# Optimization experiments

Hardware: AMD Instinct MI355X
Metric: run time of the kernel (lower is better)

Reference implementation:

```python
import jax, jax.numpy as jnp
import numpy as np

N_DOCS, DOC_LEN, H = 10000, 200, 128   # document token vectors [N, d, h]
B, QLEN, NPIDS = 16, 32, 500           # batch, query tokens, candidate pids per query
TOPK = 100


def setup_inputs() -> dict:
    key = jax.random.key(0)
    k1, k2, k3 = jax.random.split(key, 3)
    q_vectors = jax.random.normal(k1, (B, QLEN, H), dtype=jnp.float32)
    vectors = jax.random.normal(k2, (N_DOCS, DOC_LEN, H), dtype=jnp.float32)
    pids = jax.random.randint(k3, (B, NPIDS), 0, N_DOCS, dtype=jnp.int32)
    boundaries = jnp.array([0, N_DOCS], dtype=jnp.int32)
    return {"q_vectors": q_vectors, "pids": pids, "vectors": vectors,
            "boundaries": boundaries, "k": TOPK}


def _dedupe_row(row):
    # torch.unique-like: sort ascending, replace duplicate entries with -1.
    # (Original pads each row's unique set with -1; only tie-order in the
    #  downstream top-k can differ, the score/pid sets are identical.)
    s = jnp.sort(row)
    dup = jnp.concatenate([jnp.zeros((1,), dtype=bool), s[1:] == s[:-1]])
    return jnp.where(dup, jnp.int32(-1), s)


def reference(q_vectors, pids, vectors, boundaries, k):
    lo = boundaries[0]
    n_vec = vectors.shape[0]
    pids = pids - lo
    pids = jnp.where((pids < 0) | (pids >= n_vec), jnp.int32(-1), pids)
    pids = jax.vmap(_dedupe_row)(pids)                       # [b, K]

    # gather doc token vectors (pid == -1 wraps to last doc; masked below,
    # matching torch's vectors[pids] semantics for -1)
    d_vectors = vectors[pids]                                # [b, K, d, h]
    scores = jnp.einsum('bqh,bkdh->bkqd', q_vectors, d_vectors)
    scores = scores.max(axis=-1).sum(axis=-1)                # MaxSim: max over doc tokens, sum over query tokens -> [b, K]
    scores = jnp.where(pids < 0, -jnp.inf, scores)

    top_scores, top_idx = jax.lax.top_k(scores, k)           # sorted descending
    top_pids = jnp.take_along_axis(pids, top_idx, axis=-1)
    top_pids = jnp.where(top_pids >= 0, top_pids + lo, top_pids)
    return top_scores, top_pids
```

## Files before the change

### kernel.cpp

```cpp
#include <hip/hip_runtime.h>
#include <float.h>
#include <limits.h>

#define NB     16
#define QLEN   32
#define HDIM   128
#define NPIDS  500
#define NDOCS  10000
#define DLEN   200
#define TOPK   100
#define VROW   (DLEN * HDIM)

typedef _Float16 f16x8 __attribute__((ext_vector_type(8)));
typedef float    f32x16 __attribute__((ext_vector_type(16)));

__global__ __launch_bounds__(512) void dedupe_kernel(const int* __restrict__ pids,
                                                     const int* __restrict__ boundaries,
                                                     int* __restrict__ dpids) {
    __shared__ int s[512];
    const int b = blockIdx.x;
    const int t = threadIdx.x;
    const int lo = boundaries[0];

    int v = INT_MAX;
    if (t < NPIDS) {
        int p = pids[b * NPIDS + t] - lo;
        if (p < 0 || p >= NDOCS) p = -1;
        v = p;
    }
    s[t] = v;
    __syncthreads();

    for (int k = 2; k <= 512; k <<= 1) {
        for (int j = k >> 1; j > 0; j >>= 1) {
            int ixj = t ^ j;
            if (ixj > t) {
                int a = s[t], c = s[ixj];
                bool up = ((t & k) == 0);
                if ((a > c) == up) { s[t] = c; s[ixj] = a; }
            }
            __syncthreads();
        }
    }

    if (t < NPIDS) {
        int val = s[t];
        int o = val;
        if (val == INT_MAX) o = -1;
        else if (t > 0 && val == s[t - 1]) o = -1;
        dpids[b * NPIDS + t] = o;
    }
}

__device__ __forceinline__ void split2h(float a, _Float16& h, _Float16& m) {
    h = (_Float16)a;
    float r = a - (float)h;
    m = (_Float16)r;
}

__device__ __forceinline__ void split2h_pack8(const float4 c0, const float4 c1,
                                              f16x8& H, f16x8& M) {
    float f[8] = {c0.x, c0.y, c0.z, c0.w, c1.x, c1.y, c1.z, c1.w};
    f16x8 Ht, Mt;
    #pragma unroll
    for (int j = 0; j < 8; ++j) {
        _Float16 hh, mm;
        split2h(f[j], hh, mm);
        Ht[j] = hh; Mt[j] = mm;
    }
    H = Ht; M = Mt;
}

__global__ __launch_bounds__(256, 3) void score_kernel(const float* __restrict__ qv,
                                                       const float* __restrict__ vectors,
                                                       const int* __restrict__ dpids,
                                                       float* __restrict__ scores) {
    const int t    = threadIdx.x;
    const int w    = t >> 6;
    const int lane = t & 63;
    const int row  = lane & 31;
    const int half = lane >> 5;

    const int cbase = (blockIdx.x * 4 + w) * 2;
    const int b     = cbase / NPIDS;

    f16x8 qh[8], qm[8];
    {
        const float* qb = qv + ((size_t)b * QLEN + row) * HDIM + half * 8;
        #pragma unroll
        for (int ks = 0; ks < 8; ++ks) {
            const float4 a0 = *(const float4*)(qb + ks * 16);
            const float4 a1 = *(const float4*)(qb + ks * 16 + 4);
            split2h_pack8(a0, a1, qh[ks], qm[ks]);
        }
    }

    for (int ci = 0; ci < 2; ++ci) {
        const int c   = cbase + ci;
        const int pid = dpids[c];
        if (pid < 0) {
            if (lane == 0) scores[c] = -__builtin_inff();
            continue;
        }

        const float* vb = vectors + (size_t)pid * VROW + half * 8;

        float rmax[16];
        #pragma unroll
        for (int j = 0; j < 16; ++j) rmax[j] = -FLT_MAX;

        const float* vt0 = vb + (size_t)row * HDIM;
        float4 pf[4][2];
        #pragma unroll
        for (int s = 0; s < 4; ++s) {
            pf[s][0] = *(const float4*)(vt0 + s * 16);
            pf[s][1] = *(const float4*)(vt0 + s * 16 + 4);
        }

        #pragma unroll 1
        for (int tile = 0; tile < 7; ++tile) {
            int tok = tile * 32 + row;
            if (tok > DLEN - 1) tok = DLEN - 1;
            const float* vt = vb + (size_t)tok * HDIM;
            int tokn = (tile + 1) * 32 + row;
            if (tokn > DLEN - 1) tokn = DLEN - 1;
            const float* vtn = vb + (size_t)tokn * HDIM;

            f32x16 acc;
            #pragma unroll
            for (int j = 0; j < 16; ++j) acc[j] = 0.0f;

            #pragma unroll
            for (int ks = 0; ks < 8; ++ks) {
                const int slot = ks & 3;
                const float4 c0 = pf[slot][0];
                const float4 c1 = pf[slot][1];

                if (ks < 4) {
                    pf[slot][0] = *(const float4*)(vt + (ks + 4) * 16);
                    pf[slot][1] = *(const float4*)(vt + (ks + 4) * 16 + 4);
                } else if (tile < 6) {
                    pf[slot][0] = *(const float4*)(vtn + (ks - 4) * 16);
                    pf[slot][1] = *(const float4*)(vtn + (ks - 4) * 16 + 4);
                }

                f16x8 vh, vm;
                split2h_pack8(c0, c1, vh, vm);
                acc = __builtin_amdgcn_mfma_f32_32x32x16_f16(qh[ks], vh, acc, 0, 0, 0);
                acc = __builtin_amdgcn_mfma_f32_32x32x16_f16(qh[ks], vm, acc, 0, 0, 0);
                acc = __builtin_amdgcn_mfma_f32_32x32x16_f16(qm[ks], vh, acc, 0, 0, 0);
            }

            #pragma unroll
            for (int j = 0; j < 16; ++j) rmax[j] = fmaxf(rmax[j], acc[j]);
        }

        double dsum = 0.0;
        #pragma unroll
        for (int j = 0; j < 16; ++j) {
            float m = rmax[j];
            m = fmaxf(m, __shfl_xor(m, 1));
            m = fmaxf(m, __shfl_xor(m, 2));
            m = fmaxf(m, __shfl_xor(m, 4));
            m = fmaxf(m, __shfl_xor(m, 8));
            m = fmaxf(m, __shfl_xor(m, 16));
            dsum += (double)m;
        }
        dsum += __shfl_xor(dsum, 32);
        if (lane == 0) scores[c] = (float)dsum;
    }
}

__global__ __launch_bounds__(512) void topk_kernel(const float* __restrict__ scores,
                                                   const int* __restrict__ dpids,
                                                   const int* __restrict__ boundaries,
                                                   float* __restrict__ out) {
    __shared__ float ss[512];
    __shared__ int   sp[512];
    const int b = blockIdx.x;
    const int t = threadIdx.x;
    const int lo = boundaries[0];

    float sc = -__builtin_inff();
    int   p  = -1;
    if (t < NPIDS) {
        p = dpids[b * NPIDS + t];
        sc = (p < 0) ? -__builtin_inff() : scores[b * NPIDS + t];
    }
    ss[t] = sc;
    sp[t] = p;
    __syncthreads();

    for (int k = 2; k <= 512; k <<= 1) {
        for (int j = k >> 1; j > 0; j >>= 1) {
            int ixj = t ^ j;
            if (ixj > t) {
                float a = ss[t], c = ss[ixj];
                bool down = ((t & k) == 0);
                bool swap = down ? (a < c) : (a > c);
                if (swap) {
                    int pa = sp[t], pc = sp[ixj];
                    ss[t] = c;   ss[ixj] = a;
                    sp[t] = pc;  sp[ixj] = pa;
                }
            }
            __syncthreads();
        }
    }

    if (t < TOPK) {
        out[b * TOPK + t] = ss[t];
        int pp = sp[t];
        out[NB * TOPK + b * TOPK + t] = (pp >= 0) ? (float)(pp + lo) : -1.0f;
    }
}

extern "C" void kernel_launch(void* const* d_in, const int* in_sizes, int n_in,
                              void* d_out, int out_size, void* d_ws, size_t ws_size,
                              hipStream_t stream) {
    const float* qv        = (const float*)d_in[0];
    const int*   pids      = (const int*)d_in[1];
    const float* vectors   = (const float*)d_in[2];
    const int*   boundaries= (const int*)d_in[3];

    int*   dpids  = (int*)d_ws;
    float* scores = (float*)((char*)d_ws + 32768);

    dedupe_kernel<<<NB, 512, 0, stream>>>(pids, boundaries, dpids);
    score_kernel <<<(NB * NPIDS) / 8, 256, 0, stream>>>(qv, vectors, dpids, scores);
    topk_kernel  <<<NB, 512, 0, stream>>>(scores, dpids, boundaries, (float*)d_out);
}
```

Baseline: 173.2 us.

## Stream doc vectors through an LDS ring via async global_load_lds

Replaces the per-lane register prefetch of document token vectors with a 4-unit shared-memory ring filled by global_load_lds direct-to-LDS loads. Reads use an XOR swizzle, and explicit vmcnt waits keep several units in flight while the MFMA work runs. Blocks shrink from 256 threads to one 64-lane wave, with 32 KB of LDS per block. The goal is more memory-level parallelism and less register pressure on the bandwidth-bound gather. The cost is lower occupancy from the LDS footprint and fragile hand-tuned waitcnt counts.

After: 168.0 us. -3.0%, faster.

```diff
diff --git a/kernel.cpp b/kernel.cpp
--- a/kernel.cpp
+++ b/kernel.cpp
@@ -10,6 +10,10 @@
 #define DLEN   200
 #define TOPK   100
 #define VROW   (DLEN * HDIM)
+
+#define UNIT_BYTES 8192
+#define RING_UNITS 4
+#define NUNITS     14
 
 typedef _Float16 f16x8 __attribute__((ext_vector_type(8)));
 typedef float    f32x16 __attribute__((ext_vector_type(16)));
@@ -71,18 +75,17 @@
     H = Ht; M = Mt;
 }
 
-__global__ __launch_bounds__(256, 3) void score_kernel(const float* __restrict__ qv,
-                                                       const float* __restrict__ vectors,
-                                                       const int* __restrict__ dpids,
-                                                       float* __restrict__ scores) {
-    const int t    = threadIdx.x;
-    const int w    = t >> 6;
-    const int lane = t & 63;
+__global__ __launch_bounds__(64) void score_kernel(const float* __restrict__ qv,
+                                                   const float* __restrict__ vectors,
+                                                   const int* __restrict__ dpids,
+                                                   float* __restrict__ scores) {
+    const int lane = threadIdx.x;
     const int row  = lane & 31;
     const int half = lane >> 5;
-
-    const int cbase = (blockIdx.x * 4 + w) * 2;
+    const int cbase = blockIdx.x * 2;
     const int b     = cbase / NPIDS;
+
+    __shared__ __align__(16) unsigned char ring[RING_UNITS * UNIT_BYTES];
 
     f16x8 qh[8], qm[8];
     {
@@ -94,6 +97,7 @@
             split2h_pack8(a0, a1, qh[ks], qm[ks]);
         }
     }
+    __builtin_amdgcn_sched_barrier(0);
 
     for (int ci = 0; ci < 2; ++ci) {
         const int c   = cbase + ci;
@@ -103,47 +107,55 @@
             continue;
         }
 
-        const float* vb = vectors + (size_t)pid * VROW + half * 8;
+        const char* vcand = (const char*)(vectors + (size_t)pid * VROW);
+
+        auto stage = [&](int u) {
+            const int tile = u >> 1, seg = u & 1;
+            const int sbase = (u & 3) * UNIT_BYTES;
+            #pragma unroll
+            for (int i = 0; i < 8; ++i) {
+                const int p  = i * 1024 + lane * 16;
+                const int tp = p >> 8;
+                int tg = tile * 32 + tp;
+                if (tg > DLEN - 1) tg = DLEN - 1;
+                const unsigned soff = (unsigned)tg * 512u + (unsigned)seg * 256u
+                                    + (unsigned)((p & 255) ^ ((tp & 7) << 4));
+                __builtin_amdgcn_global_load_lds(
+                    (const __attribute__((address_space(1))) void*)(vcand + soff),
+                    (__attribute__((address_space(3))) void*)(&ring[sbase + i * 1024]),
+                    16, 0, 0);
+            }
+        };
 
         float rmax[16];
         #pragma unroll
         for (int j = 0; j < 16; ++j) rmax[j] = -FLT_MAX;
 
-        const float* vt0 = vb + (size_t)row * HDIM;
-        float4 pf[4][2];
-        #pragma unroll
-        for (int s = 0; s < 4; ++s) {
-            pf[s][0] = *(const float4*)(vt0 + s * 16);
-            pf[s][1] = *(const float4*)(vt0 + s * 16 + 4);
-        }
-
-        #pragma unroll 1
-        for (int tile = 0; tile < 7; ++tile) {
-            int tok = tile * 32 + row;
-            if (tok > DLEN - 1) tok = DLEN - 1;
-            const float* vt = vb + (size_t)tok * HDIM;
-            int tokn = (tile + 1) * 32 + row;
-            if (tokn > DLEN - 1) tokn = DLEN - 1;
-            const float* vtn = vb + (size_t)tokn * HDIM;
-
-            f32x16 acc;
+        f32x16 acc;
+
+        stage(0); stage(1); stage(2); stage(3);
+
+        #pragma unroll
+        for (int u = 0; u < NUNITS; ++u) {
+            if (u <= 10)      asm volatile("s_waitcnt vmcnt(24)" ::: "memory");
+            else if (u == 11) asm volatile("s_waitcnt vmcnt(16)" ::: "memory");
+            else if (u == 12) asm volatile("s_waitcnt vmcnt(8)"  ::: "memory");
+            else              asm volatile("s_waitcnt vmcnt(0)"  ::: "memory");
+
+            if ((u & 1) == 0) {
+                #pragma unroll
+                for (int j = 0; j < 16; ++j) acc[j] = 0.0f;
+            }
+
+            const int ubase = (u & 3) * UNIT_BYTES;
+            const int seg   = u & 1;
+            const int swz   = (row & 7) << 4;
             #pragma unroll
-            for (int j = 0; j < 16; ++j) acc[j] = 0.0f;
-
-            #pragma unroll
-            for (int ks = 0; ks < 8; ++ks) {
-                const int slot = ks & 3;
-                const float4 c0 = pf[slot][0];
-                const float4 c1 = pf[slot][1];
-
-                if (ks < 4) {
-                    pf[slot][0] = *(const float4*)(vt + (ks + 4) * 16);
-                    pf[slot][1] = *(const float4*)(vt + (ks + 4) * 16 + 4);
-                } else if (tile < 6) {
-                    pf[slot][0] = *(const float4*)(vtn + (ks - 4) * 16);
-                    pf[slot][1] = *(const float4*)(vtn + (ks - 4) * 16 + 4);
-                }
-
+            for (int k2 = 0; k2 < 4; ++k2) {
+                const int ks   = seg * 4 + k2;
+                const int off0 = row * 256 + k2 * 64 + half * 32;
+                const float4 c0 = *(const float4*)&ring[ubase + (off0 ^ swz)];
+                const float4 c1 = *(const float4*)&ring[ubase + ((off0 + 16) ^ swz)];
                 f16x8 vh, vm;
                 split2h_pack8(c0, c1, vh, vm);
                 acc = __builtin_amdgcn_mfma_f32_32x32x16_f16(qh[ks], vh, acc, 0, 0, 0);
@@ -151,8 +163,13 @@
                 acc = __builtin_amdgcn_mfma_f32_32x32x16_f16(qm[ks], vh, acc, 0, 0, 0);
             }
 
-            #pragma unroll
-            for (int j = 0; j < 16; ++j) rmax[j] = fmaxf(rmax[j], acc[j]);
+            if (u & 1) {
+                #pragma unroll
+                for (int j = 0; j < 16; ++j) rmax[j] = fmaxf(rmax[j], acc[j]);
+            }
+
+            __builtin_amdgcn_sched_barrier(0);
+            if (u + 4 < NUNITS) stage(u + 4);
         }
 
         double dsum = 0.0;
@@ -227,6 +244,6 @@
     float* scores = (float*)((char*)d_ws + 32768);
 
     dedupe_kernel<<<NB, 512, 0, stream>>>(pids, boundaries, dpids);
-    score_kernel <<<(NB * NPIDS) / 8, 256, 0, stream>>>(qv, vectors, dpids, scores);
+    score_kernel <<<(NB * NPIDS) / 2, 64, 0, stream>>>(qv, vectors, dpids, scores);
     topk_kernel  <<<NB, 512, 0, stream>>>(scores, dpids, boundaries, (float*)d_out);
 }
```
